# Performance work log

Hardware: AMD Instinct MI355X
Metric: run time of the kernel (lower is better)

## Reference

```python
import jax, jax.numpy as jnp
import numpy as np

N = 2048        # nodes
IN_DIM = 128    # input feature dim
K = 8           # channels
D = 32          # per-channel dim (C_dim)
ITERS = 4       # routing iterations
BETA = 1.0      # attention temperature
EPS = 1e-12     # F.normalize eps


def l2norm(x):
    # F.normalize(x, dim=-1): x / max(||x||_2, eps)
    n = jnp.linalg.norm(x, axis=-1, keepdims=True)
    return x / jnp.maximum(n, EPS)


def setup_inputs() -> dict:
    key = jax.random.key(0)
    k1, k2, k3, k4 = jax.random.split(key, 4)
    adj = jax.random.randint(k1, (N, N), 0, 2, dtype=jnp.int32)
    features = jax.random.normal(k2, (N, IN_DIM), dtype=jnp.float32)
    # parameters initialized ~ N(0,1) as in init_parameters
    W = jax.random.normal(k3, (K, IN_DIM, D), dtype=jnp.float32)
    b = jax.random.normal(k4, (K, D), dtype=jnp.float32)
    return {"adj": adj, "features": features, "W": W, "b": b}


def reference(adj, features, W, b):
    mask = (adj > 0)[None, :, :]                         # [1, N, N]
    # per-channel projection + row L2 normalize -> Z: [K, N, D]
    Z = l2norm(jnp.einsum('nd,kdc->knc', features, W) + b[:, None, :])
    for _ in range(ITERS):
        # per-channel masked attention scores [K, N, N]
        att = jnp.einsum('knc,kmc->knm', Z, Z)
        att = jnp.where(mask, att, 0.0) / BETA
        # softmax across channels (dim=2 in torch after cat == K axis here)
        att = jax.nn.softmax(att, axis=0)
        att = jnp.where(mask, att, 0.0)
        # weighted aggregate + residual + L2 normalize
        Z = l2norm(Z + jnp.einsum('knm,kmc->knc', att, Z))
    # concat channels along feature dim -> [N, K*D]
    return jnp.transpose(Z, (1, 0, 2)).reshape(N, K * D)
```

## Files before the change

### kernel.cpp

```cpp
#include <hip/hip_runtime.h>
#include <hip/hip_bf16.h>

#define NN 2048
#define KK 8
#define DD 32
#define ZSZ (KK * NN * DD)
#define PSTR 36

#define TW(row, slot) (((row) << 4) + ((((slot) ^ (((row) >> 1) & 3))) << 2))

typedef __attribute__((ext_vector_type(8))) short short8;
typedef __attribute__((ext_vector_type(4))) float f32x4;
typedef __attribute__((ext_vector_type(4))) unsigned int u32x4;

union UU { u32x4 q; short8 v; unsigned int u[4]; };

#define SELHI 0x07060302u
#define SELLO 0x05040100u

__device__ __forceinline__ unsigned int prm(unsigned int a, unsigned int b, unsigned int sel) {
  return __builtin_amdgcn_perm(a, b, sel);
}
__device__ __forceinline__ unsigned int bfr(float x) {
  unsigned int u = __float_as_uint(x);
  return (u + 0x7fffu + ((u >> 16) & 1u)) >> 16;
}
__device__ __forceinline__ unsigned int packp(float a, float b) {
  union { __hip_bfloat162 h; unsigned int u; } cv;
  cv.h = __float22bfloat162_rn(make_float2(a, b));
  return cv.u;
}
__device__ __forceinline__ f32x4 MF(short8 a, short8 b, f32x4 c) {
  return __builtin_amdgcn_mfma_f32_16x16x32_bf16(a, b, c, 0, 0, 0);
}
__device__ __forceinline__ short8 as_s8(u32x4 x) { UU u; u.q = x; return u.v; }

__global__ __launch_bounds__(256) void pm_kernel(const float* __restrict__ feat,
                                                 const float* __restrict__ W,
                                                 const float* __restrict__ bias,
                                                 float* __restrict__ Z,
                                                 unsigned short* __restrict__ Zghi,
                                                 unsigned short* __restrict__ Zthi,
                                                 const int* __restrict__ adj,
                                                 unsigned int* __restrict__ mbits) {
  const int t = threadIdx.x;
  if (blockIdx.x < 256) {
    const int nb = blockIdx.x * 8;
    const int k = t >> 5, c = t & 31;
    float s[8];
#pragma unroll
    for (int j = 0; j < 8; ++j) s[j] = bias[k * DD + c];
    const float* w = W + (k * 128) * DD + c;
    const float* fp = feat + nb * 128;
#pragma unroll 4
    for (int d = 0; d < 128; ++d) {
      float wv = w[d * DD];
#pragma unroll
      for (int j = 0; j < 8; ++j) s[j] = fmaf(fp[j * 128 + d], wv, s[j]);
    }
    unsigned int hi[8];
#pragma unroll
    for (int j = 0; j < 8; ++j) {
      float sq = s[j] * s[j];
#pragma unroll
      for (int off = 16; off > 0; off >>= 1) sq += __shfl_xor(sq, off, 32);
      float z = s[j] / fmaxf(sqrtf(sq), 1e-12f);
      Z[(k * NN + nb + j) * DD + c] = z;
      hi[j] = bfr(z);
      Zghi[(k * NN + nb + j) * DD + c] = (unsigned short)hi[j];
    }
    uint4 tp = make_uint4(hi[0] | (hi[1] << 16), hi[2] | (hi[3] << 16),
                          hi[4] | (hi[5] << 16), hi[6] | (hi[7] << 16));
    *(uint4*)&Zthi[(size_t)k * DD * NN + (size_t)c * NN + nb] = tp;
  } else {
    const int base = (blockIdx.x - 256) * 1024 + t;
    const int lane = t & 63;
    int v[4];
#pragma unroll
    for (int rr = 0; rr < 4; ++rr) v[rr] = adj[base + 256 * rr];
#pragma unroll
    for (int rr = 0; rr < 4; ++rr) {
      int idx = base + 256 * rr;
      unsigned long long b = __ballot(v[rr] > 0);
      if (lane == 0) mbits[idx >> 5] = (unsigned int)b;
      if (lane == 32) mbits[idx >> 5] = (unsigned int)(b >> 32);
    }
  }
}

template <int NCt>
__global__ __launch_bounds__(256) void rp_kernel(const float* __restrict__ Zin,
                                                 const float* __restrict__ part,
                                                 float* __restrict__ Zout,
                                                 unsigned short* __restrict__ Zghi,
                                                 unsigned short* __restrict__ Zthi) {
  __shared__ unsigned short T[DD][33];
  const int t = threadIdx.x;
  const int k = blockIdx.x >> 6, mt = blockIdx.x & 63;
  const int m0 = mt * 32;
  const int mloc = t >> 3, c4 = t & 7;
  const size_t idx = (size_t)(k * NN + m0 + mloc) * DD + 4 * c4;
  float4 v = *(const float4*)&Zin[idx];
#pragma unroll
  for (int j = 0; j < NCt; ++j) {
    float4 p = *(const float4*)&part[(size_t)j * ZSZ + idx];
    v.x += p.x; v.y += p.y; v.z += p.z; v.w += p.w;
  }
  float sq = v.x * v.x + v.y * v.y + v.z * v.z + v.w * v.w;
  sq += __shfl_xor(sq, 1, 8);
  sq += __shfl_xor(sq, 2, 8);
  sq += __shfl_xor(sq, 4, 8);
  const float sc = 1.0f / fmaxf(sqrtf(sq), 1e-12f);
  float z[4] = {v.x * sc, v.y * sc, v.z * sc, v.w * sc};
  *(float4*)&Zout[idx] = make_float4(z[0], z[1], z[2], z[3]);
  unsigned int hi[4];
#pragma unroll
  for (int e = 0; e < 4; ++e) {
    hi[e] = bfr(z[e]);
    T[4 * c4 + e][mloc] = (unsigned short)hi[e];
  }
  *(uint2*)&Zghi[idx] = make_uint2(hi[0] | (hi[1] << 16), hi[2] | (hi[3] << 16));
  __syncthreads();
  const int cloc = t >> 3, m4 = t & 7;
  unsigned int o0 = (unsigned int)T[cloc][4 * m4 + 0] | ((unsigned int)T[cloc][4 * m4 + 1] << 16);
  unsigned int o1 = (unsigned int)T[cloc][4 * m4 + 2] | ((unsigned int)T[cloc][4 * m4 + 3] << 16);
  *(uint2*)&Zthi[(size_t)k * DD * NN + (size_t)cloc * NN + m0 + 4 * m4] = make_uint2(o0, o1);
}

template <int NS>
__global__ __launch_bounds__(256, 2) void iter_kernel(const unsigned short* __restrict__ Zghi,
                                                      const unsigned short* __restrict__ Zthi,
                                                      const unsigned int* __restrict__ mbits,
                                                      float* __restrict__ part) {
  __shared__ __align__(16) unsigned int lds[8192 + 4 * 4 * 16 * PSTR];
  const int t = threadIdx.x;
  const int w = t >> 6;
  const int lane = t & 63;
  const int l15 = lane & 15;
  const int g = lane >> 4;
  const int nw = blockIdx.x * 64 + w * 16;
  const int mchunk = blockIdx.y * (NS * 32);

  const unsigned int* Zg = (const unsigned int*)Zghi;
  const unsigned int* Zt = (const unsigned int*)Zthi;

  short8 A[KK];
#pragma unroll
  for (int k = 0; k < KK; ++k)
    A[k] = as_s8(*(const u32x4*)&Zg[(size_t)(k * NN + nw + l15) * 16 + 4 * g]);

  unsigned int mwa[4][NS];
#pragma unroll
  for (int r = 0; r < 4; ++r)
#pragma unroll
    for (int q4 = 0; q4 < NS / 4; ++q4) {
      uint4 m4 = *(const uint4*)&mbits[(size_t)(nw + 4 * g + r) * 64 + (mchunk >> 5) + 4 * q4];
      mwa[r][4 * q4 + 0] = m4.x; mwa[r][4 * q4 + 1] = m4.y;
      mwa[r][4 * q4 + 2] = m4.z; mwa[r][4 * q4 + 3] = m4.w;
    }

  f32x4 O[KK][2];
#pragma unroll
  for (int k = 0; k < KK; ++k)
#pragma unroll
    for (int ch = 0; ch < 2; ++ch) O[k][ch] = {0.0f, 0.0f, 0.0f, 0.0f};

  const int sqd = t & 3;
  const int sr0 = t >> 2;

  u32x4 Lgh[4], Lth[4];
  auto do_loads = [&](int mb) {
#pragma unroll
    for (int j = 0; j < 4; ++j) {
      int r = 64 * j + sr0;
      int k = r >> 5, rm = r & 31;
      Lgh[j] = *(const u32x4*)&Zg[(size_t)k * (NN * 16) + (size_t)(mb + rm) * 16 + sqd * 4];
      Lth[j] = *(const u32x4*)&Zt[(size_t)k * (NN * 16) + (size_t)rm * (NN / 2) + (mb >> 1) + sqd * 4];
    }
  };
  do_loads(mchunk);

  unsigned int* Pw = &lds[8192 + w * (4 * 16 * PSTR)];

#pragma unroll
  for (int st = 0; st < NS; ++st) {
    const int mb = mchunk + st * 32;
    __syncthreads();
#pragma unroll
    for (int j = 0; j < 4; ++j) {
      int r = 64 * j + sr0;
      *(u32x4*)&lds[TW(r, sqd)] = Lgh[j];
      *(u32x4*)&lds[4096 + TW(r, sqd)] = Lth[j];
    }
    __syncthreads();
    if (st + 1 < NS) do_loads(mb + 32);

#pragma unroll
    for (int sub = 0; sub < 2; ++sub) {
      f32x4 S[KK];
#pragma unroll
      for (int k = 0; k < KK; ++k) {
        int row = k * 32 + 16 * sub + l15;
        u32x4 bh = *(const u32x4*)&lds[TW(row, g)];
        f32x4 z = {0.0f, 0.0f, 0.0f, 0.0f};
        S[k] = MF(A[k], as_s8(bh), z);
      }
#pragma unroll
      for (int r = 0; r < 4; ++r) {
        float e[KK];
        float sum = 0.0f;
#pragma unroll
        for (int k = 0; k < KK; ++k) { e[k] = __expf(S[k][r]); sum += e[k]; }
        int ml = 16 * sub + l15;
        float f = ((mwa[r][st] >> ml) & 1u) ? __builtin_amdgcn_rcpf(sum) : 0.0f;
#pragma unroll
        for (int k = 0; k < KK; ++k) S[k][r] = e[k] * f;
      }
#pragma unroll
      for (int kp = 0; kp < 4; ++kp)
#pragma unroll
        for (int r = 0; r < 4; ++r) {
          int n = 4 * g + r;
          Pw[kp * (16 * PSTR) + n * PSTR + 16 * sub + l15] =
              packp(S[2 * kp][r], S[2 * kp + 1][r]);
        }
    }

#pragma unroll
    for (int kp = 0; kp < 4; ++kp) {
      const unsigned int* Pr = &Pw[kp * (16 * PSTR) + l15 * PSTR + 8 * g];
      u32x4 a0 = *(const u32x4*)Pr;
      u32x4 a1 = *(const u32x4*)(Pr + 4);
      UU pk0, pk1;
      pk0.u[0] = prm(a0.y, a0.x, SELLO); pk0.u[1] = prm(a0.w, a0.z, SELLO);
      pk0.u[2] = prm(a1.y, a1.x, SELLO); pk0.u[3] = prm(a1.w, a1.z, SELLO);
      pk1.u[0] = prm(a0.y, a0.x, SELHI); pk1.u[1] = prm(a0.w, a0.z, SELHI);
      pk1.u[2] = prm(a1.y, a1.x, SELHI); pk1.u[3] = prm(a1.w, a1.z, SELHI);
#pragma unroll
      for (int kk = 0; kk < 2; ++kk) {
        int k = 2 * kp + kk;
#pragma unroll
        for (int ch = 0; ch < 2; ++ch) {
          int row = k * 32 + 16 * ch + l15;
          u32x4 b = *(const u32x4*)&lds[4096 + TW(row, g)];
          O[k][ch] = MF(kk ? pk1.v : pk0.v, as_s8(b), O[k][ch]);
        }
      }
    }
  }

  float* dst = part + (size_t)blockIdx.y * ZSZ;
#pragma unroll
  for (int k = 0; k < KK; ++k)
#pragma unroll
    for (int ch = 0; ch < 2; ++ch) {
      f32x4 o = O[k][ch];
#pragma unroll
      for (int r = 0; r < 4; ++r)
        dst[(size_t)(k * NN + nw + 4 * g + r) * DD + 16 * ch + l15] = o[r];
    }
}

template <int NCt>
__global__ __launch_bounds__(256) void ro_kernel(const float* __restrict__ Zin,
                                                 const float* __restrict__ part,
                                                 float* __restrict__ out) {
  const int n = blockIdx.x, t = threadIdx.x;
  const int k = t >> 5, c = t & 31;
  const size_t idx = (size_t)(k * NN + n) * DD + c;
  float v = Zin[idx];
#pragma unroll
  for (int j = 0; j < NCt; ++j) v += part[(size_t)j * ZSZ + idx];
  float sq = v * v;
#pragma unroll
  for (int off = 16; off > 0; off >>= 1) sq += __shfl_xor(sq, off, 32);
  out[n * (KK * DD) + t] = v / fmaxf(sqrtf(sq), 1e-12f);
}

extern "C" void kernel_launch(void* const* d_in, const int* in_sizes, int n_in,
                              void* d_out, int out_size, void* d_ws, size_t ws_size,
                              hipStream_t stream) {
  const int* adj = (const int*)d_in[0];
  const float* feat = (const float*)d_in[1];
  const float* W = (const float*)d_in[2];
  const float* b = (const float*)d_in[3];
  float* out = (float*)d_out;

  int NC = 16;
  while (NC > 4) {
    size_t need = ((size_t)ZSZ * (2 + NC) + NN * 64) * 4 + (size_t)ZSZ * 2 * 2;
    if (need <= ws_size) break;
    NC >>= 1;
  }

  float* Z0 = (float*)d_ws;
  float* Z1 = Z0 + ZSZ;
  unsigned short* Zghi = (unsigned short*)(Z1 + ZSZ);
  unsigned short* Zthi = Zghi + ZSZ;
  unsigned int* mbits = (unsigned int*)(Zthi + ZSZ);
  float* part = (float*)(mbits + NN * 64);

  pm_kernel<<<256 + 4096, 256, 0, stream>>>(feat, W, b, Z0, Zghi, Zthi, adj, mbits);

  float* zi = Z0;
  float* zo = Z1;
  for (int it = 0; it < 4; ++it) {
    if (NC == 16)
      iter_kernel<4><<<dim3(32, 16), 256, 0, stream>>>(Zghi, Zthi, mbits, part);
    else if (NC == 8)
      iter_kernel<8><<<dim3(32, 8), 256, 0, stream>>>(Zghi, Zthi, mbits, part);
    else
      iter_kernel<16><<<dim3(32, 4), 256, 0, stream>>>(Zghi, Zthi, mbits, part);
    if (it < 3) {
      if (NC == 16)
        rp_kernel<16><<<512, 256, 0, stream>>>(zi, part, zo, Zghi, Zthi);
      else if (NC == 8)
        rp_kernel<8><<<512, 256, 0, stream>>>(zi, part, zo, Zghi, Zthi);
      else
        rp_kernel<4><<<512, 256, 0, stream>>>(zi, part, zo, Zghi, Zthi);
      float* tmp = zi; zi = zo; zo = tmp;
    } else {
      if (NC == 16)
        ro_kernel<16><<<NN, 256, 0, stream>>>(zi, part, out);
      else if (NC == 8)
        ro_kernel<8><<<NN, 256, 0, stream>>>(zi, part, out);
      else
        ro_kernel<4><<<NN, 256, 0, stream>>>(zi, part, out);
    }
  }
}
```

Measured before the change: 195.4 us.

## Store partial sums in fp16 and drop fp32 Z copies in favor of bf16

Iteration partial outputs are written as fp16 instead of fp32, halving the bytes written by iter_kernel and read by the reduction kernels. The separate fp32 Z buffers are removed, and the residual term is reconstructed from the bf16 Z copy already kept for the MFMA inputs. This cuts global memory traffic and workspace size. The cost is extra rounding in both the residual and the partial aggregates, which may accumulate across iterations.

```diff
diff --git a/kernel.cpp b/kernel.cpp
--- a/kernel.cpp
+++ b/kernel.cpp
@@ -1,5 +1,6 @@
 #include <hip/hip_runtime.h>
 #include <hip/hip_bf16.h>
+#include <hip/hip_fp16.h>
 
 #define NN 2048
 #define KK 8
@@ -25,6 +26,9 @@
   unsigned int u = __float_as_uint(x);
   return (u + 0x7fffu + ((u >> 16) & 1u)) >> 16;
 }
+__device__ __forceinline__ float bf2f(unsigned int h) {
+  return __uint_as_float(h << 16);
+}
 __device__ __forceinline__ unsigned int packp(float a, float b) {
   union { __hip_bfloat162 h; unsigned int u; } cv;
   cv.h = __float22bfloat162_rn(make_float2(a, b));
@@ -38,7 +42,6 @@
 __global__ __launch_bounds__(256) void pm_kernel(const float* __restrict__ feat,
                                                  const float* __restrict__ W,
                                                  const float* __restrict__ bias,
-                                                 float* __restrict__ Z,
                                                  unsigned short* __restrict__ Zghi,
                                                  unsigned short* __restrict__ Zthi,
                                                  const int* __restrict__ adj,
@@ -65,7 +68,6 @@
 #pragma unroll
       for (int off = 16; off > 0; off >>= 1) sq += __shfl_xor(sq, off, 32);
       float z = s[j] / fmaxf(sqrtf(sq), 1e-12f);
-      Z[(k * NN + nb + j) * DD + c] = z;
       hi[j] = bfr(z);
       Zghi[(k * NN + nb + j) * DD + c] = (unsigned short)hi[j];
     }
@@ -89,9 +91,7 @@
 }
 
 template <int NCt>
-__global__ __launch_bounds__(256) void rp_kernel(const float* __restrict__ Zin,
-                                                 const float* __restrict__ part,
-                                                 float* __restrict__ Zout,
+__global__ __launch_bounds__(256) void rp_kernel(const __half* __restrict__ part,
                                                  unsigned short* __restrict__ Zghi,
                                                  unsigned short* __restrict__ Zthi) {
   __shared__ unsigned short T[DD][33];
@@ -100,11 +100,18 @@
   const int m0 = mt * 32;
   const int mloc = t >> 3, c4 = t & 7;
   const size_t idx = (size_t)(k * NN + m0 + mloc) * DD + 4 * c4;
-  float4 v = *(const float4*)&Zin[idx];
+  uint2 zb = *(const uint2*)&Zghi[idx];
+  float4 v;
+  v.x = bf2f(zb.x & 0xffffu);
+  v.y = __uint_as_float(zb.x & 0xffff0000u);
+  v.z = bf2f(zb.y & 0xffffu);
+  v.w = __uint_as_float(zb.y & 0xffff0000u);
 #pragma unroll
   for (int j = 0; j < NCt; ++j) {
-    float4 p = *(const float4*)&part[(size_t)j * ZSZ + idx];
-    v.x += p.x; v.y += p.y; v.z += p.z; v.w += p.w;
+    const __half2* ph = (const __half2*)&part[(size_t)j * ZSZ + idx];
+    float2 a = __half22float2(ph[0]);
+    float2 b = __half22float2(ph[1]);
+    v.x += a.x; v.y += a.y; v.z += b.x; v.w += b.y;
   }
   float sq = v.x * v.x + v.y * v.y + v.z * v.z + v.w * v.w;
   sq += __shfl_xor(sq, 1, 8);
@@ -112,7 +119,6 @@
   sq += __shfl_xor(sq, 4, 8);
   const float sc = 1.0f / fmaxf(sqrtf(sq), 1e-12f);
   float z[4] = {v.x * sc, v.y * sc, v.z * sc, v.w * sc};
-  *(float4*)&Zout[idx] = make_float4(z[0], z[1], z[2], z[3]);
   unsigned int hi[4];
 #pragma unroll
   for (int e = 0; e < 4; ++e) {
@@ -131,7 +137,7 @@
 __global__ __launch_bounds__(256, 2) void iter_kernel(const unsigned short* __restrict__ Zghi,
                                                       const unsigned short* __restrict__ Zthi,
                                                       const unsigned int* __restrict__ mbits,
-                                                      float* __restrict__ part) {
+                                                      __half* __restrict__ part) {
   __shared__ __align__(16) unsigned int lds[8192 + 4 * 4 * 16 * PSTR];
   const int t = threadIdx.x;
   const int w = t >> 6;
@@ -249,7 +255,7 @@
     }
   }
 
-  float* dst = part + (size_t)blockIdx.y * ZSZ;
+  __half* dst = part + (size_t)blockIdx.y * ZSZ;
 #pragma unroll
   for (int k = 0; k < KK; ++k)
 #pragma unroll
@@ -257,20 +263,20 @@
       f32x4 o = O[k][ch];
 #pragma unroll
       for (int r = 0; r < 4; ++r)
-        dst[(size_t)(k * NN + nw + 4 * g + r) * DD + 16 * ch + l15] = o[r];
+        dst[(size_t)(k * NN + nw + 4 * g + r) * DD + 16 * ch + l15] = __float2half_rn(o[r]);
     }
 }
 
 template <int NCt>
-__global__ __launch_bounds__(256) void ro_kernel(const float* __restrict__ Zin,
-                                                 const float* __restrict__ part,
+__global__ __launch_bounds__(256) void ro_kernel(const unsigned short* __restrict__ Zghi,
+                                                 const __half* __restrict__ part,
                                                  float* __restrict__ out) {
   const int n = blockIdx.x, t = threadIdx.x;
   const int k = t >> 5, c = t & 31;
   const size_t idx = (size_t)(k * NN + n) * DD + c;
-  float v = Zin[idx];
-#pragma unroll
-  for (int j = 0; j < NCt; ++j) v += part[(size_t)j * ZSZ + idx];
+  float v = bf2f((unsigned int)Zghi[idx]);
+#pragma unroll
+  for (int j = 0; j < NCt; ++j) v += __half2float(part[(size_t)j * ZSZ + idx]);
   float sq = v * v;
 #pragma unroll
   for (int off = 16; off > 0; off >>= 1) sq += __shfl_xor(sq, off, 32);
@@ -288,22 +294,18 @@
 
   int NC = 16;
   while (NC > 4) {
-    size_t need = ((size_t)ZSZ * (2 + NC) + NN * 64) * 4 + (size_t)ZSZ * 2 * 2;
+    size_t need = (size_t)ZSZ * 2 * 2 + (size_t)NN * 64 * 4 + (size_t)NC * ZSZ * 2;
     if (need <= ws_size) break;
     NC >>= 1;
   }
 
-  float* Z0 = (float*)d_ws;
-  float* Z1 = Z0 + ZSZ;
-  unsigned short* Zghi = (unsigned short*)(Z1 + ZSZ);
+  unsigned short* Zghi = (unsigned short*)d_ws;
   unsigned short* Zthi = Zghi + ZSZ;
   unsigned int* mbits = (unsigned int*)(Zthi + ZSZ);
-  float* part = (float*)(mbits + NN * 64);
-
-  pm_kernel<<<256 + 4096, 256, 0, stream>>>(feat, W, b, Z0, Zghi, Zthi, adj, mbits);
-
-  float* zi = Z0;
-  float* zo = Z1;
+  __half* part = (__half*)(mbits + NN * 64);
+
+  pm_kernel<<<256 + 4096, 256, 0, stream>>>(feat, W, b, Zghi, Zthi, adj, mbits);
+
   for (int it = 0; it < 4; ++it) {
     if (NC == 16)
       iter_kernel<4><<<dim3(32, 16), 256, 0, stream>>>(Zghi, Zthi, mbits, part);
@@ -313,19 +315,18 @@
       iter_kernel<16><<<dim3(32, 4), 256, 0, stream>>>(Zghi, Zthi, mbits, part);
     if (it < 3) {
       if (NC == 16)
-        rp_kernel<16><<<512, 256, 0, stream>>>(zi, part, zo, Zghi, Zthi);
+        rp_kernel<16><<<512, 256, 0, stream>>>(part, Zghi, Zthi);
       else if (NC == 8)
-        rp_kernel<8><<<512, 256, 0, stream>>>(zi, part, zo, Zghi, Zthi);
+        rp_kernel<8><<<512, 256, 0, stream>>>(part, Zghi, Zthi);
       else
-        rp_kernel<4><<<512, 256, 0, stream>>>(zi, part, zo, Zghi, Zthi);
-      float* tmp = zi; zi = zo; zo = tmp;
+        rp_kernel<4><<<512, 256, 0, stream>>>(part, Zghi, Zthi);
     } else {
       if (NC == 16)
-        ro_kernel<16><<<NN, 256, 0, stream>>>(zi, part, out);
+        ro_kernel<16><<<NN, 256, 0, stream>>>(Zghi, part, out);
       else if (NC == 8)
-        ro_kernel<8><<<NN, 256, 0, stream>>>(zi, part, out);
+        ro_kernel<8><<<NN, 256, 0, stream>>>(Zghi, part, out);
       else
-        ro_kernel<4><<<NN, 256, 0, stream>>>(zi, part, out);
-    }
-  }
-}
+        ro_kernel<4><<<NN, 256, 0, stream>>>(Zghi, part, out);
+    }
+  }
+}
```

Result: faster. 189.1 us (-3.3%).
